# Performance work log

Measured on AMD Instinct MI355X. Metric: run time of the kernel, lower is better.

The kernel has to match this reference:

```python
import jax, jax.numpy as jnp
import numpy as np

BATCH = 4096
IN_F = 1024
OUT_F = 1024
GRID_SIZE = 8
SPLINE_ORDER = 3
SCALE_SPLINE = 1.0


def setup_inputs() -> dict:
    key = jax.random.key(0)
    kx, kb, ks = jax.random.split(key, 3)
    # inputs live on the spline domain [-1, 1]
    x = jax.random.uniform(kx, (BATCH, IN_F), jnp.float32, -1.0, 1.0)
    # kaiming_uniform_(a=sqrt(5)) on (out,in) -> U(-1/sqrt(in), 1/sqrt(in))
    bound = 1.0 / float(np.sqrt(IN_F))
    base_weight = jax.random.uniform(kb, (OUT_F, IN_F), jnp.float32, -bound, bound)
    # normal(mean=0, std=0.1), (out, in, grid_size + spline_order)
    spline_weight = 0.1 * jax.random.normal(ks, (OUT_F, IN_F, GRID_SIZE + SPLINE_ORDER), jnp.float32)
    # uniform knot vector with spacing h = 2/grid_size over [-1,1], extended by
    # spline_order knots on each side so Cox-de Boor yields grid_size+spline_order bases
    h = 2.0 / GRID_SIZE
    grid = jnp.arange(-SPLINE_ORDER, GRID_SIZE + SPLINE_ORDER + 1, dtype=jnp.float32) * h - 1.0
    return {"x": x, "base_weight": base_weight, "spline_weight": spline_weight, "grid": grid}


def b_spline_basis(x, grid, k):
    # x: (batch, in), grid: (grid_size + 2k + 1,) shared across (out, in) pairs
    xe = x[..., None]  # (b, i, 1)
    # degree-0: indicator of knot interval -> (b, i, grid_size + 2k)
    basis = ((xe >= grid[:-1]) & (xe < grid[1:])).astype(x.dtype)
    for d in range(1, k + 1):  # Cox-de Boor recursion up to degree k
        left_denom = grid[d:-1] - grid[:-(d + 1)]
        right_denom = grid[d + 1:] - grid[1:-d]
        left_denom = jnp.where(left_denom > 0, left_denom, 1.0)
        right_denom = jnp.where(right_denom > 0, right_denom, 1.0)
        basis = ((xe - grid[:-(d + 1)]) / left_denom * basis[..., :-1]
                 + (grid[d + 1:] - xe) / right_denom * basis[..., 1:])
    return basis  # (b, i, grid_size + k)


def reference(x, base_weight, spline_weight, grid):
    base_output = x @ base_weight.T  # (b, out)
    basis = b_spline_basis(x, grid, SPLINE_ORDER)  # (b, i, L), L = grid_size + k
    # grid is identical for every (out, in) pair, so the per-(o,i) basis of the
    # original collapses to a per-i basis; einsum 'bil,oil->bo' is the same math.
    spline_output = jnp.einsum('bil,oil->bo', basis, spline_weight)
    return base_output + SCALE_SPLINE * spline_output
```

## Files before the change

kernel.cpp:

```cpp
#include <hip/hip_runtime.h>
#include <hip/hip_bf16.h>
#include <cstdint>

#define BATCH 4096
#define INF   1024
#define OUTF  1024
#define LCH   12
#define KTOT  (INF*LCH)
#define KHALF (KTOT/2)
#define IHALF (INF/2)

#define BM 128
#define BN 128
#define IC 4
#define BK (IC*LCH)
#define NCHUNK (IHALF/IC)
#define NGRAN (BK/8)
#define THREADS 256
#define BUFSZ (NGRAN*128*8)

#define WT_BYTES   ((size_t)OUTF * KTOT * 2)
#define OUT_BYTES  ((size_t)BATCH * OUTF * 4)

typedef __bf16 bf16x8 __attribute__((ext_vector_type(8)));
typedef float  f32x16 __attribute__((ext_vector_type(16)));
typedef unsigned long long ull;

struct alignas(16) U2 { ull x, y; };

__device__ __forceinline__ unsigned short f2bf(float f) {
  unsigned int u = __builtin_bit_cast(unsigned int, f);
  u += 0x7FFFu + ((u >> 16) & 1u);
  return (unsigned short)(u >> 16);
}

__device__ __forceinline__ void async_copy16(const void* g, void* l) {
  __builtin_amdgcn_global_load_lds(
      (const __attribute__((address_space(1))) unsigned int*)g,
      (__attribute__((address_space(3))) unsigned int*)l,
      16, 0, 0);
}

#define PIPE_BARRIER() do {                                        \
  asm volatile("s_waitcnt vmcnt(4) lgkmcnt(0)" ::: "memory");      \
  __builtin_amdgcn_sched_barrier(0);                               \
  __builtin_amdgcn_s_barrier();                                    \
  __builtin_amdgcn_sched_barrier(0);                               \
} while (0)

__global__ __launch_bounds__(256) void kan_build_wt(
    const float* __restrict__ sw,
    const float* __restrict__ bw,
    unsigned short* __restrict__ Wt)
{
  int idx = blockIdx.x * 256 + threadIdx.x;
  int o = idx >> 10;
  int i = idx & 1023;
  const float* s = sw + (size_t)(o * 1024 + i) * 11;
  unsigned short v[12];
#pragma unroll
  for (int l = 0; l < 11; ++l) v[l] = f2bf(s[l]);
  v[11] = f2bf(bw[o * 1024 + i]);
  unsigned short* d = Wt + (size_t)o * KTOT + i * 12;
  *reinterpret_cast<ushort4*>(d + 0) = make_ushort4(v[0], v[1], v[2],  v[3]);
  *reinterpret_cast<ushort4*>(d + 4) = make_ushort4(v[4], v[5], v[6],  v[7]);
  *reinterpret_cast<ushort4*>(d + 8) = make_ushort4(v[8], v[9], v[10], v[11]);
}

template <bool USE_ATOMIC>
__global__ __launch_bounds__(THREADS, 2) void kan_gemm(
    const float* __restrict__ x,
    const unsigned short* __restrict__ Wt,
    float* __restrict__ out,
    float* __restrict__ partial)
{
  __shared__ alignas(16) unsigned short smem[5 * BUFSZ];

  const int tid  = threadIdx.x;
  const int lane = tid & 63;
  const int wid  = tid >> 6;
  const int qm   = wid >> 1;
  const int qn   = wid & 1;
  const int lo   = lane & 31;
  const int lh   = lane >> 5;
  const int idx  = (int)blockIdx.x;
  const int bn   = idx & 7;
  const int kh   = (idx >> 3) & 1;
  const int bm   = idx >> 4;

  const int ab  = tid & 127;
  const int ai0 = (tid >> 7) << 1;
  const float* xrow = x + (size_t)(bm * BM + ab) * INF + kh * IHALF + ai0;
  const size_t kbase = (size_t)kh * KHALF;

  unsigned short* Bcur = smem;
  unsigned short* Bnxt = smem + BUFSZ;
  unsigned short* Bnn  = smem + 2 * BUFSZ;
  unsigned short* Acur = smem + 3 * BUFSZ;
  unsigned short* Aalt = smem + 4 * BUFSZ;

  f32x16 acc[2][2] = {};

  auto stageB = [&](int c, unsigned short* Bd) {
#pragma unroll
    for (int qq = 0; qq < 3; ++qq) {
      int G  = (wid * 3 + qq) * 64 + lane;
      int kk = G >> 7;
      int oo = G & 127;
      const unsigned short* src =
          Wt + (size_t)(bn * BN + oo) * KTOT + kbase + c * BK + kk * 8;
      async_copy16(src, Bd + (wid * 3 + qq) * 512);
    }
  };

  auto buildA = [&](float2 xv, unsigned short* Ad) {
    ull W[6];
#pragma unroll
    for (int j = 0; j < 2; ++j) {
      float xx = (j == 0) ? xv.x : xv.y;
      float u  = fmaf(xx, 4.0f, 7.0f);
      float fm = floorf(u);
      int   mi = (int)fm;
      float t  = u - fm;
      float s  = 1.0f - t;
      float t2 = t * t, t3 = t2 * t;
      float w0 = (s * s * s) * (1.0f / 6.0f);
      float w3 = t3 * (1.0f / 6.0f);
      float w1 = fmaf(0.5f, t3, 2.0f / 3.0f) - t2;
      float w2 = 1.0f - w0 - w1 - w3;
      int ls = mi - 3;

      ull W64 = (ull)f2bf(w0)
              | ((ull)f2bf(w1) << 16)
              | ((ull)f2bf(w2) << 32)
              | ((ull)f2bf(w3) << 48);
      int sh = ls << 4;
      int a  = sh & 63;
      ull lop  = W64 << a;
      ull hip_ = a ? (W64 >> (64 - a)) : 0ull;
      W[3 * j + 0] = (sh < 64) ? lop : 0ull;
      W[3 * j + 1] = (sh < 64) ? hip_ : lop;
      W[3 * j + 2] = ((sh < 64) ? 0ull : hip_) | ((ull)f2bf(xx) << 48);
    }
    U2* p = reinterpret_cast<U2*>(Ad);
    const int g0 = (ai0 >> 1) * 3;
    U2 u0; u0.x = W[0]; u0.y = W[1];
    U2 u1; u1.x = W[2]; u1.y = W[3];
    U2 u2; u2.x = W[4]; u2.y = W[5];
    p[(g0 + 0) * 128 + ab] = u0;
    p[(g0 + 1) * 128 + ab] = u1;
    p[(g0 + 2) * 128 + ab] = u2;
  };

  float2 x0v = *reinterpret_cast<const float2*>(xrow);
  stageB(0, Bcur);
  buildA(x0v, Acur);
  float2 xa = *reinterpret_cast<const float2*>(xrow + IC);
  stageB(1, Bnxt);
  PIPE_BARRIER();

  for (int c = 0; c < NCHUNK; ++c) {
    int cf = (c + 2 < NCHUNK) ? (c + 2) : (NCHUNK - 1);
    float2 xb = *reinterpret_cast<const float2*>(xrow + cf * IC);
    stageB(cf, Bnn);
    buildA(xa, Aalt);

#pragma unroll
    for (int s = 0; s < 3; ++s) {
      const int kk = s * 2 + lh;
      bf16x8 af0 = *reinterpret_cast<const bf16x8*>(&Acur[(kk * 128 + qm * 64 + lo) * 8]);
      bf16x8 af1 = *reinterpret_cast<const bf16x8*>(&Acur[(kk * 128 + qm * 64 + 32 + lo) * 8]);
      bf16x8 bf0 = *reinterpret_cast<const bf16x8*>(&Bcur[(kk * 128 + qn * 64 + lo) * 8]);
      bf16x8 bf1 = *reinterpret_cast<const bf16x8*>(&Bcur[(kk * 128 + qn * 64 + 32 + lo) * 8]);
      acc[0][0] = __builtin_amdgcn_mfma_f32_32x32x16_bf16(af0, bf0, acc[0][0], 0, 0, 0);
      acc[0][1] = __builtin_amdgcn_mfma_f32_32x32x16_bf16(af0, bf1, acc[0][1], 0, 0, 0);
      acc[1][0] = __builtin_amdgcn_mfma_f32_32x32x16_bf16(af1, bf0, acc[1][0], 0, 0, 0);
      acc[1][1] = __builtin_amdgcn_mfma_f32_32x32x16_bf16(af1, bf1, acc[1][1], 0, 0, 0);
    }

    PIPE_BARRIER();

    unsigned short* t = Bcur; Bcur = Bnxt; Bnxt = Bnn; Bnn = t;
    t = Acur; Acur = Aalt; Aalt = t;
    xa = xb;
  }

  asm volatile("s_waitcnt vmcnt(0) lgkmcnt(0)" ::: "memory");

  float* dst = (USE_ATOMIC || kh == 0) ? out : partial;
#pragma unroll
  for (int mf = 0; mf < 2; ++mf) {
#pragma unroll
    for (int r = 0; r < 16; ++r) {
      int row = bm * BM + qm * 64 + mf * 32 + (r & 3) + 8 * (r >> 2) + 4 * lh;
      float* orow = dst + (size_t)row * OUTF + bn * BN + qn * 64 + lo;
#pragma unroll
      for (int nf = 0; nf < 2; ++nf) {
        if (USE_ATOMIC) atomicAdd(&orow[nf * 32], acc[mf][nf][r]);
        else            orow[nf * 32] = acc[mf][nf][r];
      }
    }
  }
}

__global__ __launch_bounds__(256) void kan_reduce(
    float4* __restrict__ out, const float4* __restrict__ p)
{
  int i = blockIdx.x * 256 + threadIdx.x;
  float4 a = out[i], b = p[i];
  a.x += b.x; a.y += b.y; a.z += b.z; a.w += b.w;
  out[i] = a;
}

extern "C" void kernel_launch(void* const* d_in, const int* in_sizes, int n_in,
                              void* d_out, int out_size, void* d_ws, size_t ws_size,
                              hipStream_t stream) {
  const float* x  = (const float*)d_in[0];
  const float* bw = (const float*)d_in[1];
  const float* sw = (const float*)d_in[2];
  float* out = (float*)d_out;

  unsigned short* Wt = (unsigned short*)d_ws;
  if (ws_size < WT_BYTES) return;

  kan_build_wt<<<(OUTF * INF) / 256, 256, 0, stream>>>(sw, bw, Wt);

  if (ws_size >= WT_BYTES + OUT_BYTES) {
    float* partial = (float*)((char*)d_ws + WT_BYTES);
    kan_gemm<false><<<512, THREADS, 0, stream>>>(x, Wt, out, partial);
    kan_reduce<<<(BATCH * OUTF / 4) / 256, 256, 0, stream>>>(
        (float4*)out, (const float4*)partial);
  } else {
    hipMemsetAsync(d_out, 0, OUT_BYTES, stream);
    kan_gemm<true><<<512, THREADS, 0, stream>>>(x, Wt, out, out);
  }
}
```

Baseline: 172.6 us.

## Specialize warps into A-builders and B-stagers with 512-thread GEMM blocks

```diff
diff --git a/kernel.cpp b/kernel.cpp
--- a/kernel.cpp
+++ b/kernel.cpp
@@ -16,7 +16,7 @@
 #define BK (IC*LCH)
 #define NCHUNK (IHALF/IC)
 #define NGRAN (BK/8)
-#define THREADS 256
+#define THREADS 512
 #define BUFSZ (NGRAN*128*8)
 
 #define WT_BYTES   ((size_t)OUTF * KTOT * 2)
@@ -42,7 +42,7 @@
 }
 
 #define PIPE_BARRIER() do {                                        \
-  asm volatile("s_waitcnt vmcnt(4) lgkmcnt(0)" ::: "memory");      \
+  asm volatile("s_waitcnt vmcnt(3) lgkmcnt(0)" ::: "memory");      \
   __builtin_amdgcn_sched_barrier(0);                               \
   __builtin_amdgcn_s_barrier();                                    \
   __builtin_amdgcn_sched_barrier(0);                               \
@@ -68,7 +68,7 @@
 }
 
 template <bool USE_ATOMIC>
-__global__ __launch_bounds__(THREADS, 2) void kan_gemm(
+__global__ __launch_bounds__(THREADS, 4) void kan_gemm(
     const float* __restrict__ x,
     const unsigned short* __restrict__ Wt,
     float* __restrict__ out,
@@ -79,17 +79,19 @@
   const int tid  = threadIdx.x;
   const int lane = tid & 63;
   const int wid  = tid >> 6;
-  const int qm   = wid >> 1;
-  const int qn   = wid & 1;
+  const int wm   = (wid >> 2) * 64;
+  const int wn   = (wid & 3) * 32;
   const int lo   = lane & 31;
   const int lh   = lane >> 5;
   const int idx  = (int)blockIdx.x;
   const int bn   = idx & 7;
   const int kh   = (idx >> 3) & 1;
   const int bm   = idx >> 4;
+  const bool builder = (tid < 256);
+  const bool stager  = (wid >= 4);
 
   const int ab  = tid & 127;
-  const int ai0 = (tid >> 7) << 1;
+  const int ai0 = ((tid >> 7) & 1) << 1;
   const float* xrow = x + (size_t)(bm * BM + ab) * INF + kh * IHALF + ai0;
   const size_t kbase = (size_t)kh * KHALF;
 
@@ -99,17 +101,18 @@
   unsigned short* Acur = smem + 3 * BUFSZ;
   unsigned short* Aalt = smem + 4 * BUFSZ;
 
-  f32x16 acc[2][2] = {};
+  f32x16 acc[2] = {};
 
   auto stageB = [&](int c, unsigned short* Bd) {
+    const int wq = wid - 4;
 #pragma unroll
     for (int qq = 0; qq < 3; ++qq) {
-      int G  = (wid * 3 + qq) * 64 + lane;
+      int G  = (wq * 3 + qq) * 64 + lane;
       int kk = G >> 7;
       int oo = G & 127;
       const unsigned short* src =
           Wt + (size_t)(bn * BN + oo) * KTOT + kbase + c * BK + kk * 8;
-      async_copy16(src, Bd + (wid * 3 + qq) * 512);
+      async_copy16(src, Bd + (wq * 3 + qq) * 512);
     }
   };
 
@@ -130,10 +133,11 @@
       float w2 = 1.0f - w0 - w1 - w3;
       int ls = mi - 3;
 
-      ull W64 = (ull)f2bf(w0)
-              | ((ull)f2bf(w1) << 16)
-              | ((ull)f2bf(w2) << 32)
-              | ((ull)f2bf(w3) << 48);
+      unsigned int p01, p23;
+      asm("v_cvt_pk_bf16_f32 %0, %1, %2" : "=v"(p01) : "v"(w0), "v"(w1));
+      asm("v_cvt_pk_bf16_f32 %0, %1, %2" : "=v"(p23) : "v"(w2), "v"(w3));
+      ull W64 = (ull)p01 | ((ull)p23 << 32);
+
       int sh = ls << 4;
       int a  = sh & 63;
       ull lop  = W64 << a;
@@ -152,30 +156,35 @@
     p[(g0 + 2) * 128 + ab] = u2;
   };
 
-  float2 x0v = *reinterpret_cast<const float2*>(xrow);
-  stageB(0, Bcur);
-  buildA(x0v, Acur);
-  float2 xa = *reinterpret_cast<const float2*>(xrow + IC);
-  stageB(1, Bnxt);
+  float2 xa = make_float2(0.f, 0.f);
+  if (builder) {
+    float2 x0v = *reinterpret_cast<const float2*>(xrow);
+    buildA(x0v, Acur);
+    xa = *reinterpret_cast<const float2*>(xrow + IC);
+  }
+  if (stager) {
+    stageB(0, Bcur);
+    stageB(1, Bnxt);
+  }
   PIPE_BARRIER();
 
   for (int c = 0; c < NCHUNK; ++c) {
     int cf = (c + 2 < NCHUNK) ? (c + 2) : (NCHUNK - 1);
-    float2 xb = *reinterpret_cast<const float2*>(xrow + cf * IC);
-    stageB(cf, Bnn);
-    buildA(xa, Aalt);
+    float2 xb = xa;
+    if (builder) {
+      xb = *reinterpret_cast<const float2*>(xrow + cf * IC);
+      buildA(xa, Aalt);
+    }
+    if (stager) stageB(cf, Bnn);
 
 #pragma unroll
     for (int s = 0; s < 3; ++s) {
       const int kk = s * 2 + lh;
-      bf16x8 af0 = *reinterpret_cast<const bf16x8*>(&Acur[(kk * 128 + qm * 64 + lo) * 8]);
-      bf16x8 af1 = *reinterpret_cast<const bf16x8*>(&Acur[(kk * 128 + qm * 64 + 32 + lo) * 8]);
-      bf16x8 bf0 = *reinterpret_cast<const bf16x8*>(&Bcur[(kk * 128 + qn * 64 + lo) * 8]);
-      bf16x8 bf1 = *reinterpret_cast<const bf16x8*>(&Bcur[(kk * 128 + qn * 64 + 32 + lo) * 8]);
-      acc[0][0] = __builtin_amdgcn_mfma_f32_32x32x16_bf16(af0, bf0, acc[0][0], 0, 0, 0);
-      acc[0][1] = __builtin_amdgcn_mfma_f32_32x32x16_bf16(af0, bf1, acc[0][1], 0, 0, 0);
-      acc[1][0] = __builtin_amdgcn_mfma_f32_32x32x16_bf16(af1, bf0, acc[1][0], 0, 0, 0);
-      acc[1][1] = __builtin_amdgcn_mfma_f32_32x32x16_bf16(af1, bf1, acc[1][1], 0, 0, 0);
+      bf16x8 a0 = *reinterpret_cast<const bf16x8*>(&Acur[(kk * 128 + wm + lo) * 8]);
+      bf16x8 a1 = *reinterpret_cast<const bf16x8*>(&Acur[(kk * 128 + wm + 32 + lo) * 8]);
+      bf16x8 b0 = *reinterpret_cast<const bf16x8*>(&Bcur[(kk * 128 + wn + lo) * 8]);
+      acc[0] = __builtin_amdgcn_mfma_f32_32x32x16_bf16(a0, b0, acc[0], 0, 0, 0);
+      acc[1] = __builtin_amdgcn_mfma_f32_32x32x16_bf16(a1, b0, acc[1], 0, 0, 0);
     }
 
     PIPE_BARRIER();
@@ -192,13 +201,10 @@
   for (int mf = 0; mf < 2; ++mf) {
 #pragma unroll
     for (int r = 0; r < 16; ++r) {
-      int row = bm * BM + qm * 64 + mf * 32 + (r & 3) + 8 * (r >> 2) + 4 * lh;
-      float* orow = dst + (size_t)row * OUTF + bn * BN + qn * 64 + lo;
-#pragma unroll
-      for (int nf = 0; nf < 2; ++nf) {
-        if (USE_ATOMIC) atomicAdd(&orow[nf * 32], acc[mf][nf][r]);
-        else            orow[nf * 32] = acc[mf][nf][r];
-      }
+      int row = bm * BM + wm + mf * 32 + (r & 3) + 8 * (r >> 2) + 4 * lh;
+      float* po = dst + (size_t)row * OUTF + bn * BN + wn + lo;
+      if (USE_ATOMIC) atomicAdd(po, acc[mf][r]);
+      else            *po = acc[mf][r];
     }
   }
 }
```

Result: faster. 168.6 us (-2.3%).
